# Kernel optimization log

Measured on AMD Instinct MI355X. Metric: run time of the kernel, lower is better.

The kernel has to match this reference:

```python
import jax, jax.numpy as jnp
import numpy as np

B, T, D, H = 2, 2048, 1024, 16
DH = D // H  # 64, rope dim


def rotate_half(x):
    x1, x2 = jnp.split(x, 2, axis=-1)
    return jnp.concatenate([-x2, x1], axis=-1)


def rope_tables(seq_len, dim, dtype=jnp.float32):
    inv_freq = 1.0 / (10000.0 ** (jnp.arange(0, dim, 2, dtype=jnp.float32) / dim))
    t = jnp.arange(seq_len, dtype=jnp.float32)
    freqs = jnp.outer(t, inv_freq)              # [T, dim/2]
    emb = jnp.concatenate([freqs, freqs], -1)   # [T, dim]
    return jnp.cos(emb).astype(dtype), jnp.sin(emb).astype(dtype)


def setup_inputs() -> dict:
    key = jax.random.key(0)
    ks = jax.random.split(key, 5)
    w_scale = 0.02
    x = jax.random.normal(ks[0], (B, T, D), jnp.float32)
    W_q = jax.random.normal(ks[1], (D, D), jnp.float32) * w_scale
    W_k = jax.random.normal(ks[2], (D, D), jnp.float32) * w_scale
    W_v = jax.random.normal(ks[3], (D, D), jnp.float32) * w_scale
    W_o = jax.random.normal(ks[4], (D, D), jnp.float32) * w_scale
    mask = jnp.tril(jnp.ones((T, T), jnp.int32))  # causal
    return {"x": x, "W_q": W_q, "W_k": W_k, "W_v": W_v, "W_o": W_o, "mask": mask}


def reference(x, W_q, W_k, W_v, W_o, mask):
    b, t, d = x.shape
    # Linear (bias=False): y = x @ W^T, weight shape (out, in)
    def proj(W):
        y = jnp.einsum('btd,ed->bte', x, W)
        return y.reshape(b, t, H, DH).transpose(0, 2, 1, 3)  # [B,H,T,dh]
    q, k, v = proj(W_q), proj(W_k), proj(W_v)

    cos, sin = rope_tables(t, DH, x.dtype)
    cos = cos[None, None]  # [1,1,T,dh]
    sin = sin[None, None]
    q = q * cos + rotate_half(q) * sin
    k = k * cos + rotate_half(k) * sin

    scale = 1.0 / np.sqrt(DH).astype(np.float32)
    scores = jnp.einsum('bhqd,bhkd->bhqk', q, k) * scale  # [B,H,T,T]
    neg_inf = jnp.finfo(scores.dtype).min
    scores = jnp.where(mask[:t, :t][None, None] == 0, neg_inf, scores)
    attn = jax.nn.softmax(scores, axis=-1)
    out = jnp.einsum('bhqk,bhkd->bhqd', attn, v)
    out = out.transpose(0, 2, 1, 3).reshape(b, t, d)
    return jnp.einsum('btd,ed->bte', out, W_o)
```

## Files before the change

kernel.cpp:

```cpp
#include <hip/hip_runtime.h>
#include <hip/hip_bf16.h>
#include <math.h>

#define B_  2
#define T_  2048
#define D_  1024
#define H_  16
#define DH_ 64
#define WN_ (D_ * D_)

typedef __attribute__((ext_vector_type(8))) short bf16x8;
typedef __attribute__((ext_vector_type(4))) float f32x4;
typedef __attribute__((ext_vector_type(16))) float f32x16;

__device__ __forceinline__ void gll16(const void* g, void* l) {
  __builtin_amdgcn_global_load_lds(
      (const __attribute__((address_space(1))) void*)g,
      (__attribute__((address_space(3))) void*)l, 16, 0, 0);
}

__device__ __forceinline__ void storeC(float* p, float v) { *p = v; }
__device__ __forceinline__ void storeC(__hip_bfloat16* p, float v) {
  *p = __float2bfloat16(v);
}

__global__ __launch_bounds__(256)
void cvt_f32_bf16(const float* __restrict__ in, __hip_bfloat16* __restrict__ out,
                  int n4) {
  const int i = blockIdx.x * 256 + threadIdx.x;
  if (i >= n4) return;
  const float4 a = ((const float4*)in)[i];
  __hip_bfloat16 h0 = __float2bfloat16(a.x);
  __hip_bfloat16 h1 = __float2bfloat16(a.y);
  __hip_bfloat16 h2 = __float2bfloat16(a.z);
  __hip_bfloat16 h3 = __float2bfloat16(a.w);
  ushort4 o;
  o.x = *(unsigned short*)&h0;
  o.y = *(unsigned short*)&h1;
  o.z = *(unsigned short*)&h2;
  o.w = *(unsigned short*)&h3;
  *(ushort4*)(out + (size_t)i * 4) = o;
}

__global__ __launch_bounds__(256)
void cvt3_w(const float* __restrict__ Wq, const float* __restrict__ Wk,
            const float* __restrict__ Wv, __hip_bfloat16* __restrict__ out) {
  const int i = blockIdx.x * 256 + threadIdx.x;
  const int per = WN_ / 4;
  const int sel = i >> 18;
  const int off = i & (per - 1);
  const float* src = sel == 0 ? Wq : (sel == 1 ? Wk : Wv);
  const float4 a = ((const float4*)src)[off];
  __hip_bfloat16 h0 = __float2bfloat16(a.x);
  __hip_bfloat16 h1 = __float2bfloat16(a.y);
  __hip_bfloat16 h2 = __float2bfloat16(a.z);
  __hip_bfloat16 h3 = __float2bfloat16(a.w);
  ushort4 o;
  o.x = *(unsigned short*)&h0;
  o.y = *(unsigned short*)&h1;
  o.z = *(unsigned short*)&h2;
  o.w = *(unsigned short*)&h3;
  *(ushort4*)(out + (size_t)sel * WN_ + (size_t)off * 4) = o;
}

template <typename CT>
__global__ __launch_bounds__(256)
void gemm_bf16_mfma(const __hip_bfloat16* __restrict__ A,
                    const __hip_bfloat16* __restrict__ W,
                    CT* __restrict__ C, int M, int N, int K) {
  __shared__ unsigned short As[128 * 32];
  __shared__ unsigned short Bs[128 * 32];
  const int tid = threadIdx.x;
  const int w = tid >> 6;
  const int lane = tid & 63;
  const int lg = lane >> 4;
  const int ln = lane & 15;
  const int wr = w >> 1, wc = w & 1;
  const int row0 = blockIdx.y * 128;
  const int col0 = blockIdx.x * 128;

  const int sr = w * 32 + (lane >> 2);
  const int sp = lane & 3;

  f32x4 acc[4][4];
#pragma unroll
  for (int m = 0; m < 4; ++m)
#pragma unroll
    for (int n = 0; n < 4; ++n) acc[m][n] = (f32x4){0.f, 0.f, 0.f, 0.f};

  for (int k0 = 0; k0 < K; k0 += 32) {
#pragma unroll
    for (int c = 0; c < 2; ++c) {
      const int r = sr + c * 16;
      const int ks = sp ^ ((r >> 1) & 3);
      gll16(A + (size_t)(row0 + r) * K + k0 + ks * 8,
            &As[(w * 32 + c * 16) * 32]);
      gll16(W + (size_t)(col0 + r) * K + k0 + ks * 8,
            &Bs[(w * 32 + c * 16) * 32]);
    }
    __syncthreads();

    bf16x8 af[4], bfr[4];
#pragma unroll
    for (int m = 0; m < 4; ++m) {
      const int r = wr * 64 + m * 16 + ln;
      af[m] = *(const bf16x8*)&As[r * 32 + (lg ^ ((r >> 1) & 3)) * 8];
    }
#pragma unroll
    for (int n = 0; n < 4; ++n) {
      const int r = wc * 64 + n * 16 + ln;
      bfr[n] = *(const bf16x8*)&Bs[r * 32 + (lg ^ ((r >> 1) & 3)) * 8];
    }
#pragma unroll
    for (int m = 0; m < 4; ++m)
#pragma unroll
      for (int n = 0; n < 4; ++n)
        acc[m][n] = __builtin_amdgcn_mfma_f32_16x16x32_bf16(af[m], bfr[n],
                                                            acc[m][n], 0, 0, 0);
    __syncthreads();
  }

#pragma unroll
  for (int m = 0; m < 4; ++m) {
#pragma unroll
    for (int reg = 0; reg < 4; ++reg) {
      CT* crow = C + (size_t)(row0 + wr * 64 + m * 16 + lg * 4 + reg) * N
                 + col0 + wc * 64;
#pragma unroll
      for (int n = 0; n < 4; ++n) storeC(&crow[n * 16 + ln], acc[m][n][reg]);
    }
  }
}

__global__ __launch_bounds__(256)
void rope_qkv(const __hip_bfloat16* __restrict__ qkv,
              __hip_bfloat16* __restrict__ Qb, __hip_bfloat16* __restrict__ Kb) {
  const int idx = blockIdx.x * 256 + threadIdx.x;
  const int i = idx & 31;
  const int rest = idx >> 5;
  const int row = rest >> 4;
  const int h = rest & 15;
  const int t = row & (T_ - 1);
  const float inv_freq = powf(10000.0f, -(float)i * (1.0f / 32.0f));
  const float ang = (float)t * inv_freq;
  const float c = cosf(ang), s = sinf(ang);
  const size_t rb = (size_t)row * 3072 + h * 64;
  const float q1 = __bfloat162float(qkv[rb + i]);
  const float q2 = __bfloat162float(qkv[rb + i + 32]);
  const float k1 = __bfloat162float(qkv[rb + 1024 + i]);
  const float k2 = __bfloat162float(qkv[rb + 1024 + i + 32]);
  const size_t base = (size_t)rest * DH_;
  Qb[base + i]      = __float2bfloat16((q1 * c - q2 * s) * 0.125f);
  Qb[base + i + 32] = __float2bfloat16((q2 * c + q1 * s) * 0.125f);
  Kb[base + i]      = __float2bfloat16(k1 * c - k2 * s);
  Kb[base + i + 32] = __float2bfloat16(k2 * c + k1 * s);
}

__global__ __launch_bounds__(256)
void vt_prep(const __hip_bfloat16* __restrict__ qkv,
             __hip_bfloat16* __restrict__ vt) {
  __shared__ unsigned short Ls[64][65];
  const int tt = blockIdx.x;
  const int bh = blockIdx.y;
  const int b = bh >> 4, h = bh & 15;
  const int tid = threadIdx.x;
  const int t0 = tt * 64;
  const int rb = tid >> 3, c0 = (tid & 7) * 8;
#pragma unroll
  for (int it = 0; it < 2; ++it) {
    const int r = it * 32 + rb;
    uint4 x = *(const uint4*)&qkv[(size_t)(b * T_ + t0 + r) * 3072 + 2048 +
                                  h * 64 + c0];
    const unsigned short* xs = (const unsigned short*)&x;
#pragma unroll
    for (int j = 0; j < 8; ++j) Ls[c0 + j][r] = xs[j];
  }
  __syncthreads();
  const int d = tid >> 2, t8 = (tid & 3) * 16;
  unsigned short tmp[16];
#pragma unroll
  for (int j = 0; j < 16; ++j) tmp[j] = Ls[d][t8 + j];
  __hip_bfloat16* dst = vt + ((size_t)(b * H_ + h) * 64 + d) * T_ + t0 + t8;
  *(uint4*)&dst[0] = *(uint4*)&tmp[0];
  *(uint4*)&dst[8] = *(uint4*)&tmp[8];
}

#define SWZ(row, col) ((col) ^ (((row) & 7) << 3))

__global__ __launch_bounds__(128)
void attn_mfma32(const __hip_bfloat16* __restrict__ Qb,
                 const __hip_bfloat16* __restrict__ Kb,
                 const __hip_bfloat16* __restrict__ vt,
                 __hip_bfloat16* __restrict__ O) {
  __shared__ unsigned short Ks[2][64 * 64];
  __shared__ unsigned short Vs[2][64 * 64];
  __shared__ unsigned short Ps[2][32 * 64];

  const int bx = blockIdx.x;
  const int bh = blockIdx.y;
  const int b = bh >> 4, h = bh & 15;
  const int tid = threadIdx.x;
  const int w = tid >> 6;
  const int lane = tid & 63;
  const int lq = lane & 31;
  const int hi = lane >> 5;

  const size_t headoff = (size_t)b * T_ * D_ + (size_t)h * DH_;
  const __hip_bfloat16* Qg = Qb + headoff;
  const __hip_bfloat16* Kg = Kb + headoff;
  const __hip_bfloat16* vtg = vt + (size_t)(b * H_ + h) * 64 * T_;
  __hip_bfloat16* Og = O + headoff;

  const int sr0 = tid >> 3;
  const int sc0 = (tid & 7) * 8;

  for (int pass = 0; pass < 2; ++pass) {
    const int qt = pass ? bx : 31 - bx;
    const int q_glob = qt * 64 + w * 32 + lq;

    bf16x8 qf[4];
#pragma unroll
    for (int ks = 0; ks < 4; ++ks)
      qf[ks] = *(const bf16x8*)(Qg + (size_t)q_glob * D_ + ks * 16 + hi * 8);

    uint4 kreg[4], vreg[4];
#pragma unroll
    for (int it = 0; it < 4; ++it) {
      const int r = sr0 + it * 16;
      kreg[it] = *(const uint4*)(Kg + (size_t)r * D_ + sc0);
      vreg[it] = *(const uint4*)(vtg + (size_t)r * T_ + sc0);
    }
#pragma unroll
    for (int it = 0; it < 4; ++it) {
      const int r = sr0 + it * 16;
      *(uint4*)&Ks[0][r * 64 + SWZ(r, sc0)] = kreg[it];
      *(uint4*)&Vs[0][r * 64 + SWZ(r, sc0)] = vreg[it];
    }
    if (qt >= 1) {
#pragma unroll
      for (int it = 0; it < 4; ++it) {
        const int r = sr0 + it * 16;
        kreg[it] = *(const uint4*)(Kg + (size_t)(64 + r) * D_ + sc0);
        vreg[it] = *(const uint4*)(vtg + (size_t)r * T_ + 64 + sc0);
      }
    }

    float m_run = -3.0e38f, l_run = 0.f;
    f32x16 accO[2];
#pragma unroll
    for (int reg = 0; reg < 16; ++reg) { accO[0][reg] = 0.f; accO[1][reg] = 0.f; }

    __syncthreads();

    for (int kt = 0; kt <= qt; ++kt) {
      const int buf = kt & 1;
      if (kt + 1 <= qt) {
#pragma unroll
        for (int it = 0; it < 4; ++it) {
          const int r = sr0 + it * 16;
          *(uint4*)&Ks[buf ^ 1][r * 64 + SWZ(r, sc0)] = kreg[it];
          *(uint4*)&Vs[buf ^ 1][r * 64 + SWZ(r, sc0)] = vreg[it];
        }
      }
      if (kt + 2 <= qt) {
#pragma unroll
        for (int it = 0; it < 4; ++it) {
          const int r = sr0 + it * 16;
          kreg[it] = *(const uint4*)(Kg + (size_t)((kt + 2) * 64 + r) * D_ + sc0);
          vreg[it] = *(const uint4*)(vtg + (size_t)r * T_ + (kt + 2) * 64 + sc0);
        }
      }

      f32x16 sf[2];
#pragma unroll
      for (int reg = 0; reg < 16; ++reg) { sf[0][reg] = 0.f; sf[1][reg] = 0.f; }
#pragma unroll
      for (int ks = 0; ks < 4; ++ks) {
        const int c = ks * 16 + hi * 8;
        bf16x8 ka0 = *(const bf16x8*)&Ks[buf][lq * 64 + SWZ(lq, c)];
        bf16x8 ka1 = *(const bf16x8*)&Ks[buf][(32 + lq) * 64 + SWZ(32 + lq, c)];
        sf[0] = __builtin_amdgcn_mfma_f32_32x32x16_bf16(ka0, qf[ks], sf[0], 0, 0, 0);
        sf[1] = __builtin_amdgcn_mfma_f32_32x32x16_bf16(ka1, qf[ks], sf[1], 0, 0, 0);
      }

      const int kv0 = kt * 64;
      if (kt == qt) {
#pragma unroll
        for (int reg = 0; reg < 16; ++reg) {
          const int krow = (reg & 3) + 8 * (reg >> 2) + 4 * hi;
          if (kv0 + krow > q_glob)      sf[0][reg] = -3.0e38f;
          if (kv0 + 32 + krow > q_glob) sf[1][reg] = -3.0e38f;
        }
      }

      float pmax = -3.0e38f;
#pragma unroll
      for (int reg = 0; reg < 16; ++reg)
        pmax = fmaxf(pmax, fmaxf(sf[0][reg], sf[1][reg]));
      pmax = fmaxf(pmax, __shfl_xor(pmax, 32, 64));
      const float mnew = fmaxf(m_run, pmax);
      const float alpha = __expf(m_run - mnew);
      m_run = mnew;
      float rsum = 0.f;
#pragma unroll
      for (int reg = 0; reg < 16; ++reg) {
        sf[0][reg] = __expf(sf[0][reg] - mnew);
        sf[1][reg] = __expf(sf[1][reg] - mnew);
        rsum += sf[0][reg] + sf[1][reg];
      }
      rsum += __shfl_xor(rsum, 32, 64);
      l_run = l_run * alpha + rsum;
#pragma unroll
      for (int reg = 0; reg < 16; ++reg) {
        accO[0][reg] *= alpha;
        accO[1][reg] *= alpha;
      }

#pragma unroll
      for (int kb = 0; kb < 2; ++kb) {
#pragma unroll
        for (int j = 0; j < 4; ++j) {
          __hip_bfloat16 b0 = __float2bfloat16(sf[kb][4 * j + 0]);
          __hip_bfloat16 b1 = __float2bfloat16(sf[kb][4 * j + 1]);
          __hip_bfloat16 b2 = __float2bfloat16(sf[kb][4 * j + 2]);
          __hip_bfloat16 b3 = __float2bfloat16(sf[kb][4 * j + 3]);
          uint2 pk;
          pk.x = (unsigned)*(unsigned short*)&b0 |
                 ((unsigned)*(unsigned short*)&b1 << 16);
          pk.y = (unsigned)*(unsigned short*)&b2 |
                 ((unsigned)*(unsigned short*)&b3 << 16);
          const int col = kb * 32 + 8 * j + 4 * hi;
          *(uint2*)&Ps[w][lq * 64 + SWZ(lq, col)] = pk;
        }
      }

#pragma unroll
      for (int ks = 0; ks < 4; ++ks) {
        const int c = ks * 16 + hi * 8;
        bf16x8 pb  = *(const bf16x8*)&Ps[w][lq * 64 + SWZ(lq, c)];
        bf16x8 va0 = *(const bf16x8*)&Vs[buf][lq * 64 + SWZ(lq, c)];
        bf16x8 va1 = *(const bf16x8*)&Vs[buf][(32 + lq) * 64 + SWZ(32 + lq, c)];
        accO[0] = __builtin_amdgcn_mfma_f32_32x32x16_bf16(va0, pb, accO[0], 0, 0, 0);
        accO[1] = __builtin_amdgcn_mfma_f32_32x32x16_bf16(va1, pb, accO[1], 0, 0, 0);
      }

      __syncthreads();
    }

    const float inv = 1.0f / l_run;
#pragma unroll
    for (int db = 0; db < 2; ++db) {
#pragma unroll
      for (int j = 0; j < 4; ++j) {
        __hip_bfloat16 b0 = __float2bfloat16(accO[db][4 * j + 0] * inv);
        __hip_bfloat16 b1 = __float2bfloat16(accO[db][4 * j + 1] * inv);
        __hip_bfloat16 b2 = __float2bfloat16(accO[db][4 * j + 2] * inv);
        __hip_bfloat16 b3 = __float2bfloat16(accO[db][4 * j + 3] * inv);
        uint2 pk;
        pk.x = (unsigned)*(unsigned short*)&b0 |
               ((unsigned)*(unsigned short*)&b1 << 16);
        pk.y = (unsigned)*(unsigned short*)&b2 |
               ((unsigned)*(unsigned short*)&b3 << 16);
        const int d = db * 32 + 8 * j + 4 * hi;
        *(uint2*)(Og + (size_t)q_glob * D_ + d) = pk;
      }
    }
  }
}

extern "C" void kernel_launch(void* const* d_in, const int* in_sizes, int n_in,
                              void* d_out, int out_size, void* d_ws, size_t ws_size,
                              hipStream_t stream) {
  const float* x  = (const float*)d_in[0];
  const float* Wq = (const float*)d_in[1];
  const float* Wk = (const float*)d_in[2];
  const float* Wv = (const float*)d_in[3];
  const float* Wo = (const float*)d_in[4];
  float* out = (float*)d_out;

  const size_t NE = (size_t)B_ * T_ * D_;
  char* base = (char*)d_ws;
  __hip_bfloat16* qkvb  = (__hip_bfloat16*)base;
  __hip_bfloat16* xb    = (__hip_bfloat16*)(base + 3 * NE * 2);
  __hip_bfloat16* Wqkvb = (__hip_bfloat16*)(base + 4 * NE * 2);
  __hip_bfloat16* qb    = (__hip_bfloat16*)(base + 4 * NE * 2 + 3ull * WN_ * 2);
  __hip_bfloat16* kb    = qb + NE;
  __hip_bfloat16* vtb   = kb + NE;
  __hip_bfloat16* aob   = qkvb;
  __hip_bfloat16* Wob   = Wqkvb;

  cvt_f32_bf16<<<(int)(NE / 4 / 256), 256, 0, stream>>>(x, xb, (int)(NE / 4));
  cvt3_w<<<3 * WN_ / 4 / 256, 256, 0, stream>>>(Wq, Wk, Wv, Wqkvb);

  const dim3 gq(3 * D_ / 128, (B_ * T_) / 128);
  gemm_bf16_mfma<__hip_bfloat16><<<gq, 256, 0, stream>>>(
      xb, Wqkvb, qkvb, B_ * T_, 3 * D_, D_);

  rope_qkv<<<(B_ * T_ * H_ * 32) / 256, 256, 0, stream>>>(qkvb, qb, kb);
  vt_prep<<<dim3(T_ / 64, B_ * H_), 256, 0, stream>>>(qkvb, vtb);

  const dim3 ga(T_ / 128, B_ * H_);
  attn_mfma32<<<ga, 128, 0, stream>>>(qb, kb, vtb, aob);

  cvt_f32_bf16<<<WN_ / 4 / 256, 256, 0, stream>>>(Wo, Wob, WN_ / 4);

  const dim3 go(D_ / 128, (B_ * T_) / 128);
  gemm_bf16_mfma<float><<<go, 256, 0, stream>>>(aob, Wob, out, B_ * T_, D_, D_);
}
```

Baseline: 276.7 us.

## Pre-swizzle K/V into MFMA fragment layout and stream from registers

Adds prep kernels that rewrite K and V into a per-lane MFMA fragment order, so the attention kernel loads operands straight from global memory into registers and never stages K/V through shared memory. Each wave now owns a 32-row query strip with its own causal trip count, balanced by pairing early and late strips in one 256-thread block. The kernel drops the per-tile block barrier and skips the upper half-tile MFMA on the diagonal. In exchange, each wave loads the full K/V tile on its own (no sharing across waves), and register pressure rises from double-buffered fragments.

After: 234.0 us. 1.18x faster.

```diff
diff --git a/kernel.cpp b/kernel.cpp
--- a/kernel.cpp
+++ b/kernel.cpp
@@ -157,44 +157,62 @@
 }
 
 __global__ __launch_bounds__(256)
-void vt_prep(const __hip_bfloat16* __restrict__ qkv,
-             __hip_bfloat16* __restrict__ vt) {
-  __shared__ unsigned short Ls[64][65];
-  const int tt = blockIdx.x;
+void kf_prep(const __hip_bfloat16* __restrict__ kb, __hip_bfloat16* __restrict__ Kf) {
+  const int kt = blockIdx.x;
   const int bh = blockIdx.y;
   const int b = bh >> 4, h = bh & 15;
   const int tid = threadIdx.x;
-  const int t0 = tt * 64;
+  const int j = tid & 7;
+  const int t0 = tid >> 3;
+  __hip_bfloat16* dsth = Kf + (size_t)bh * (T_ * 64) + (size_t)kt * 4096;
+#pragma unroll
+  for (int it = 0; it < 2; ++it) {
+    const int t = it * 32 + t0;
+    bf16x8 x = *(const bf16x8*)(kb +
+        (size_t)(((size_t)b * T_ + kt * 64 + t) * H_ + h) * 64 + j * 8);
+    const int kb2 = t >> 5, lane31 = t & 31, ks = j >> 1, hi = j & 1;
+    *(bf16x8*)(dsth + (((kb2 * 4 + ks) * 64 + hi * 32 + lane31) * 8)) = x;
+  }
+}
+
+__global__ __launch_bounds__(256)
+void vf_prep(const __hip_bfloat16* __restrict__ qkv, __hip_bfloat16* __restrict__ Vf) {
+  __shared__ unsigned short Ls[64][72];
+  const int kt = blockIdx.x;
+  const int bh = blockIdx.y;
+  const int b = bh >> 4, h = bh & 15;
+  const int tid = threadIdx.x;
   const int rb = tid >> 3, c0 = (tid & 7) * 8;
 #pragma unroll
   for (int it = 0; it < 2; ++it) {
     const int r = it * 32 + rb;
-    uint4 x = *(const uint4*)&qkv[(size_t)(b * T_ + t0 + r) * 3072 + 2048 +
-                                  h * 64 + c0];
+    uint4 x = *(const uint4*)&qkv[(size_t)((size_t)b * T_ + kt * 64 + r) * 3072 +
+                                  2048 + h * 64 + c0];
     const unsigned short* xs = (const unsigned short*)&x;
 #pragma unroll
-    for (int j = 0; j < 8; ++j) Ls[c0 + j][r] = xs[j];
+    for (int q = 0; q < 8; ++q) Ls[c0 + q][r] = xs[q];
   }
   __syncthreads();
-  const int d = tid >> 2, t8 = (tid & 3) * 16;
-  unsigned short tmp[16];
-#pragma unroll
-  for (int j = 0; j < 16; ++j) tmp[j] = Ls[d][t8 + j];
-  __hip_bfloat16* dst = vt + ((size_t)(b * H_ + h) * 64 + d) * T_ + t0 + t8;
-  *(uint4*)&dst[0] = *(uint4*)&tmp[0];
-  *(uint4*)&dst[8] = *(uint4*)&tmp[8];
+  __hip_bfloat16* dsth = Vf + (size_t)bh * (T_ * 64) + (size_t)kt * 4096;
+#pragma unroll
+  for (int e = 0; e < 2; ++e) {
+    const int g = e * 256 + tid;
+    const int lane31 = g & 31, hi = (g >> 5) & 1, ks = (g >> 6) & 3, kb2 = g >> 8;
+    bf16x8 x = *(const bf16x8*)&Ls[kb2 * 32 + lane31][ks * 16 + hi * 8];
+    *(bf16x8*)(dsth + (size_t)g * 8) = x;
+  }
 }
 
 #define SWZ(row, col) ((col) ^ (((row) & 7) << 3))
 
-__global__ __launch_bounds__(128)
-void attn_mfma32(const __hip_bfloat16* __restrict__ Qb,
-                 const __hip_bfloat16* __restrict__ Kb,
-                 const __hip_bfloat16* __restrict__ vt,
-                 __hip_bfloat16* __restrict__ O) {
-  __shared__ unsigned short Ks[2][64 * 64];
-  __shared__ unsigned short Vs[2][64 * 64];
-  __shared__ unsigned short Ps[2][32 * 64];
+struct KV { bf16x8 k[2][4]; bf16x8 v[2][4]; };
+
+__global__ __launch_bounds__(256, 2)
+void attn_reg(const __hip_bfloat16* __restrict__ Qb,
+              const __hip_bfloat16* __restrict__ Kf,
+              const __hip_bfloat16* __restrict__ Vf,
+              __hip_bfloat16* __restrict__ O) {
+  __shared__ unsigned short Ps[4][32 * 64];
 
   const int bx = blockIdx.x;
   const int bh = blockIdx.y;
@@ -205,165 +223,142 @@
   const int lq = lane & 31;
   const int hi = lane >> 5;
 
+  const int qu = (w < 2) ? (2 * bx + w) : (62 - 2 * bx + (w & 1));
+  const int nt = (qu >> 1) + 1;
+  const int q_glob = qu * 32 + lq;
+
   const size_t headoff = (size_t)b * T_ * D_ + (size_t)h * DH_;
   const __hip_bfloat16* Qg = Qb + headoff;
-  const __hip_bfloat16* Kg = Kb + headoff;
-  const __hip_bfloat16* vtg = vt + (size_t)(b * H_ + h) * 64 * T_;
+  const __hip_bfloat16* Kfh = Kf + (size_t)bh * (T_ * 64);
+  const __hip_bfloat16* Vfh = Vf + (size_t)bh * (T_ * 64);
   __hip_bfloat16* Og = O + headoff;
 
-  const int sr0 = tid >> 3;
-  const int sc0 = (tid & 7) * 8;
-
-  for (int pass = 0; pass < 2; ++pass) {
-    const int qt = pass ? bx : 31 - bx;
-    const int q_glob = qt * 64 + w * 32 + lq;
-
-    bf16x8 qf[4];
+  bf16x8 qf[4];
+#pragma unroll
+  for (int ks = 0; ks < 4; ++ks)
+    qf[ks] = *(const bf16x8*)(Qg + (size_t)q_glob * D_ + ks * 16 + hi * 8);
+
+  float m_run = -3.0e38f, l_run = 0.f;
+  f32x16 accO[2];
+#pragma unroll
+  for (int reg = 0; reg < 16; ++reg) { accO[0][reg] = 0.f; accO[1][reg] = 0.f; }
+
+  auto load = [&](int kt) {
+    KV r;
+    const __hip_bfloat16* kp = Kfh + (size_t)kt * 4096;
+    const __hip_bfloat16* vp = Vfh + (size_t)kt * 4096;
+#pragma unroll
+    for (int kb2 = 0; kb2 < 2; ++kb2)
+#pragma unroll
+      for (int ks = 0; ks < 4; ++ks) {
+        r.k[kb2][ks] = *(const bf16x8*)(kp + ((kb2 * 4 + ks) * 64 + lane) * 8);
+        r.v[kb2][ks] = *(const bf16x8*)(vp + ((kb2 * 4 + ks) * 64 + lane) * 8);
+      }
+    return r;
+  };
+
+  auto compute = [&](const KV& kv, int kt) {
+    f32x16 sf[2];
+#pragma unroll
+    for (int reg = 0; reg < 16; ++reg) { sf[0][reg] = 0.f; sf[1][reg] = 0.f; }
+    const bool last = (kt == nt - 1);
+    const bool skip1 = last && !(qu & 1);
 #pragma unroll
     for (int ks = 0; ks < 4; ++ks)
-      qf[ks] = *(const bf16x8*)(Qg + (size_t)q_glob * D_ + ks * 16 + hi * 8);
-
-    uint4 kreg[4], vreg[4];
-#pragma unroll
-    for (int it = 0; it < 4; ++it) {
-      const int r = sr0 + it * 16;
-      kreg[it] = *(const uint4*)(Kg + (size_t)r * D_ + sc0);
-      vreg[it] = *(const uint4*)(vtg + (size_t)r * T_ + sc0);
-    }
-#pragma unroll
-    for (int it = 0; it < 4; ++it) {
-      const int r = sr0 + it * 16;
-      *(uint4*)&Ks[0][r * 64 + SWZ(r, sc0)] = kreg[it];
-      *(uint4*)&Vs[0][r * 64 + SWZ(r, sc0)] = vreg[it];
-    }
-    if (qt >= 1) {
-#pragma unroll
-      for (int it = 0; it < 4; ++it) {
-        const int r = sr0 + it * 16;
-        kreg[it] = *(const uint4*)(Kg + (size_t)(64 + r) * D_ + sc0);
-        vreg[it] = *(const uint4*)(vtg + (size_t)r * T_ + 64 + sc0);
+      sf[0] = __builtin_amdgcn_mfma_f32_32x32x16_bf16(kv.k[0][ks], qf[ks], sf[0], 0, 0, 0);
+    if (!skip1) {
+#pragma unroll
+      for (int ks = 0; ks < 4; ++ks)
+        sf[1] = __builtin_amdgcn_mfma_f32_32x32x16_bf16(kv.k[1][ks], qf[ks], sf[1], 0, 0, 0);
+    }
+
+    if (last) {
+      const int kv0 = kt * 64;
+#pragma unroll
+      for (int reg = 0; reg < 16; ++reg) {
+        const int krow = (reg & 3) + 8 * (reg >> 2) + 4 * hi;
+        if (kv0 + krow > q_glob)      sf[0][reg] = -3.0e38f;
+        if (kv0 + 32 + krow > q_glob) sf[1][reg] = -3.0e38f;
       }
     }
 
-    float m_run = -3.0e38f, l_run = 0.f;
-    f32x16 accO[2];
-#pragma unroll
-    for (int reg = 0; reg < 16; ++reg) { accO[0][reg] = 0.f; accO[1][reg] = 0.f; }
-
-    __syncthreads();
-
-    for (int kt = 0; kt <= qt; ++kt) {
-      const int buf = kt & 1;
-      if (kt + 1 <= qt) {
-#pragma unroll
-        for (int it = 0; it < 4; ++it) {
-          const int r = sr0 + it * 16;
-          *(uint4*)&Ks[buf ^ 1][r * 64 + SWZ(r, sc0)] = kreg[it];
-          *(uint4*)&Vs[buf ^ 1][r * 64 + SWZ(r, sc0)] = vreg[it];
-        }
-      }
-      if (kt + 2 <= qt) {
-#pragma unroll
-        for (int it = 0; it < 4; ++it) {
-          const int r = sr0 + it * 16;
-          kreg[it] = *(const uint4*)(Kg + (size_t)((kt + 2) * 64 + r) * D_ + sc0);
-          vreg[it] = *(const uint4*)(vtg + (size_t)r * T_ + (kt + 2) * 64 + sc0);
-        }
-      }
-
-      f32x16 sf[2];
-#pragma unroll
-      for (int reg = 0; reg < 16; ++reg) { sf[0][reg] = 0.f; sf[1][reg] = 0.f; }
-#pragma unroll
-      for (int ks = 0; ks < 4; ++ks) {
-        const int c = ks * 16 + hi * 8;
-        bf16x8 ka0 = *(const bf16x8*)&Ks[buf][lq * 64 + SWZ(lq, c)];
-        bf16x8 ka1 = *(const bf16x8*)&Ks[buf][(32 + lq) * 64 + SWZ(32 + lq, c)];
-        sf[0] = __builtin_amdgcn_mfma_f32_32x32x16_bf16(ka0, qf[ks], sf[0], 0, 0, 0);
-        sf[1] = __builtin_amdgcn_mfma_f32_32x32x16_bf16(ka1, qf[ks], sf[1], 0, 0, 0);
-      }
-
-      const int kv0 = kt * 64;
-      if (kt == qt) {
-#pragma unroll
-        for (int reg = 0; reg < 16; ++reg) {
-          const int krow = (reg & 3) + 8 * (reg >> 2) + 4 * hi;
-          if (kv0 + krow > q_glob)      sf[0][reg] = -3.0e38f;
-          if (kv0 + 32 + krow > q_glob) sf[1][reg] = -3.0e38f;
-        }
-      }
-
-      float pmax = -3.0e38f;
-#pragma unroll
-      for (int reg = 0; reg < 16; ++reg)
-        pmax = fmaxf(pmax, fmaxf(sf[0][reg], sf[1][reg]));
-      pmax = fmaxf(pmax, __shfl_xor(pmax, 32, 64));
-      const float mnew = fmaxf(m_run, pmax);
-      const float alpha = __expf(m_run - mnew);
-      m_run = mnew;
-      float rsum = 0.f;
-#pragma unroll
-      for (int reg = 0; reg < 16; ++reg) {
-        sf[0][reg] = __expf(sf[0][reg] - mnew);
-        sf[1][reg] = __expf(sf[1][reg] - mnew);
-        rsum += sf[0][reg] + sf[1][reg];
-      }
-      rsum += __shfl_xor(rsum, 32, 64);
-      l_run = l_run * alpha + rsum;
-#pragma unroll
-      for (int reg = 0; reg < 16; ++reg) {
-        accO[0][reg] *= alpha;
-        accO[1][reg] *= alpha;
-      }
-
-#pragma unroll
-      for (int kb = 0; kb < 2; ++kb) {
-#pragma unroll
-        for (int j = 0; j < 4; ++j) {
-          __hip_bfloat16 b0 = __float2bfloat16(sf[kb][4 * j + 0]);
-          __hip_bfloat16 b1 = __float2bfloat16(sf[kb][4 * j + 1]);
-          __hip_bfloat16 b2 = __float2bfloat16(sf[kb][4 * j + 2]);
-          __hip_bfloat16 b3 = __float2bfloat16(sf[kb][4 * j + 3]);
-          uint2 pk;
-          pk.x = (unsigned)*(unsigned short*)&b0 |
-                 ((unsigned)*(unsigned short*)&b1 << 16);
-          pk.y = (unsigned)*(unsigned short*)&b2 |
-                 ((unsigned)*(unsigned short*)&b3 << 16);
-          const int col = kb * 32 + 8 * j + 4 * hi;
-          *(uint2*)&Ps[w][lq * 64 + SWZ(lq, col)] = pk;
-        }
-      }
-
-#pragma unroll
-      for (int ks = 0; ks < 4; ++ks) {
-        const int c = ks * 16 + hi * 8;
-        bf16x8 pb  = *(const bf16x8*)&Ps[w][lq * 64 + SWZ(lq, c)];
-        bf16x8 va0 = *(const bf16x8*)&Vs[buf][lq * 64 + SWZ(lq, c)];
-        bf16x8 va1 = *(const bf16x8*)&Vs[buf][(32 + lq) * 64 + SWZ(32 + lq, c)];
-        accO[0] = __builtin_amdgcn_mfma_f32_32x32x16_bf16(va0, pb, accO[0], 0, 0, 0);
-        accO[1] = __builtin_amdgcn_mfma_f32_32x32x16_bf16(va1, pb, accO[1], 0, 0, 0);
-      }
-
-      __syncthreads();
-    }
-
-    const float inv = 1.0f / l_run;
-#pragma unroll
-    for (int db = 0; db < 2; ++db) {
+    float pmax = -3.0e38f;
+#pragma unroll
+    for (int reg = 0; reg < 16; ++reg)
+      pmax = fmaxf(pmax, fmaxf(sf[0][reg], sf[1][reg]));
+    pmax = fmaxf(pmax, __shfl_xor(pmax, 32, 64));
+    const float mnew = fmaxf(m_run, pmax);
+    const float alpha = __expf(m_run - mnew);
+    m_run = mnew;
+    float rsum = 0.f;
+#pragma unroll
+    for (int reg = 0; reg < 16; ++reg) {
+      sf[0][reg] = __expf(sf[0][reg] - mnew);
+      sf[1][reg] = __expf(sf[1][reg] - mnew);
+      rsum += sf[0][reg] + sf[1][reg];
+    }
+    rsum += __shfl_xor(rsum, 32, 64);
+    l_run = l_run * alpha + rsum;
+#pragma unroll
+    for (int reg = 0; reg < 16; ++reg) {
+      accO[0][reg] *= alpha;
+      accO[1][reg] *= alpha;
+    }
+
+#pragma unroll
+    for (int kb2 = 0; kb2 < 2; ++kb2) {
 #pragma unroll
       for (int j = 0; j < 4; ++j) {
-        __hip_bfloat16 b0 = __float2bfloat16(accO[db][4 * j + 0] * inv);
-        __hip_bfloat16 b1 = __float2bfloat16(accO[db][4 * j + 1] * inv);
-        __hip_bfloat16 b2 = __float2bfloat16(accO[db][4 * j + 2] * inv);
-        __hip_bfloat16 b3 = __float2bfloat16(accO[db][4 * j + 3] * inv);
+        __hip_bfloat16 b0 = __float2bfloat16(sf[kb2][4 * j + 0]);
+        __hip_bfloat16 b1 = __float2bfloat16(sf[kb2][4 * j + 1]);
+        __hip_bfloat16 b2 = __float2bfloat16(sf[kb2][4 * j + 2]);
+        __hip_bfloat16 b3 = __float2bfloat16(sf[kb2][4 * j + 3]);
         uint2 pk;
         pk.x = (unsigned)*(unsigned short*)&b0 |
                ((unsigned)*(unsigned short*)&b1 << 16);
         pk.y = (unsigned)*(unsigned short*)&b2 |
                ((unsigned)*(unsigned short*)&b3 << 16);
-        const int d = db * 32 + 8 * j + 4 * hi;
-        *(uint2*)(Og + (size_t)q_glob * D_ + d) = pk;
+        const int col = kb2 * 32 + 8 * j + 4 * hi;
+        *(uint2*)&Ps[w][lq * 64 + SWZ(lq, col)] = pk;
       }
+    }
+
+#pragma unroll
+    for (int ks = 0; ks < 4; ++ks) {
+      const int c = ks * 16 + hi * 8;
+      bf16x8 pb = *(const bf16x8*)&Ps[w][lq * 64 + SWZ(lq, c)];
+      accO[0] = __builtin_amdgcn_mfma_f32_32x32x16_bf16(kv.v[0][ks], pb, accO[0], 0, 0, 0);
+      accO[1] = __builtin_amdgcn_mfma_f32_32x32x16_bf16(kv.v[1][ks], pb, accO[1], 0, 0, 0);
+    }
+  };
+
+  KV bufA = load(0), bufB;
+  int kt = 0;
+  while (true) {
+    if (kt + 1 < nt) bufB = load(kt + 1);
+    compute(bufA, kt);
+    ++kt; if (kt == nt) break;
+    if (kt + 1 < nt) bufA = load(kt + 1);
+    compute(bufB, kt);
+    ++kt; if (kt == nt) break;
+  }
+
+  const float inv = 1.0f / l_run;
+#pragma unroll
+  for (int db = 0; db < 2; ++db) {
+#pragma unroll
+    for (int j = 0; j < 4; ++j) {
+      __hip_bfloat16 b0 = __float2bfloat16(accO[db][4 * j + 0] * inv);
+      __hip_bfloat16 b1 = __float2bfloat16(accO[db][4 * j + 1] * inv);
+      __hip_bfloat16 b2 = __float2bfloat16(accO[db][4 * j + 2] * inv);
+      __hip_bfloat16 b3 = __float2bfloat16(accO[db][4 * j + 3] * inv);
+      uint2 pk;
+      pk.x = (unsigned)*(unsigned short*)&b0 |
+             ((unsigned)*(unsigned short*)&b1 << 16);
+      pk.y = (unsigned)*(unsigned short*)&b2 |
+             ((unsigned)*(unsigned short*)&b3 << 16);
+      const int d = db * 32 + 8 * j + 4 * hi;
+      *(uint2*)(Og + (size_t)q_glob * D_ + d) = pk;
     }
   }
 }
@@ -385,7 +380,8 @@
   __hip_bfloat16* Wqkvb = (__hip_bfloat16*)(base + 4 * NE * 2);
   __hip_bfloat16* qb    = (__hip_bfloat16*)(base + 4 * NE * 2 + 3ull * WN_ * 2);
   __hip_bfloat16* kb    = qb + NE;
-  __hip_bfloat16* vtb   = kb + NE;
+  __hip_bfloat16* Kfb   = kb + NE;
+  __hip_bfloat16* Vfb   = Kfb + NE;
   __hip_bfloat16* aob   = qkvb;
   __hip_bfloat16* Wob   = Wqkvb;
 
@@ -397,10 +393,11 @@
       xb, Wqkvb, qkvb, B_ * T_, 3 * D_, D_);
 
   rope_qkv<<<(B_ * T_ * H_ * 32) / 256, 256, 0, stream>>>(qkvb, qb, kb);
-  vt_prep<<<dim3(T_ / 64, B_ * H_), 256, 0, stream>>>(qkvb, vtb);
-
-  const dim3 ga(T_ / 128, B_ * H_);
-  attn_mfma32<<<ga, 128, 0, stream>>>(qb, kb, vtb, aob);
+  kf_prep<<<dim3(T_ / 64, B_ * H_), 256, 0, stream>>>(kb, Kfb);
+  vf_prep<<<dim3(T_ / 64, B_ * H_), 256, 0, stream>>>(qkvb, Vfb);
+
+  const dim3 ga(16, B_ * H_);
+  attn_reg<<<ga, 256, 0, stream>>>(qb, Kfb, Vfb, aob);
 
   cvt_f32_bf16<<<WN_ / 4 / 256, 256, 0, stream>>>(Wo, Wob, WN_ / 4);
 
```
